# Performance work log

Hardware: AMD Instinct MI355X
Metric: run time of the kernel (lower is better)

## Reference

```python
import jax, jax.numpy as jnp
import numpy as np

N, E, G = 50000, 600000, 256
IN_C, EMB, HID, OUT = 64, 128, 128, 36


def _glorot(key, fan_in, fan_out):
    lim = np.sqrt(6.0 / (fan_in + fan_out)).astype(np.float32)
    return jax.random.uniform(key, (fan_in, fan_out), jnp.float32, -lim, lim)


def setup_inputs() -> dict:
    key = jax.random.key(0)
    ks = jax.random.split(key, 12)
    x = jax.random.normal(ks[0], (N, IN_C), jnp.float32)
    edge_index = jax.random.randint(ks[1], (2, E), 0, N, jnp.int64)
    edge_attr = jax.random.uniform(ks[2], (E,), jnp.float32)
    # deterministic sorted batch assignment -> every graph id 0..G-1 is nonempty
    batch = ((jnp.arange(N, dtype=jnp.int64) * G) // N).astype(jnp.int64)
    rho = jax.random.uniform(ks[3], (G,), jnp.float32)
    return {
        "x": x,
        "edge_attr": edge_attr,
        "rho": rho,
        "conv0_w": _glorot(ks[4], IN_C, EMB),
        "conv0_b": jnp.zeros((EMB,), jnp.float32),
        "conv1_w": _glorot(ks[5], EMB, EMB),
        "conv1_b": jnp.zeros((EMB,), jnp.float32),
        "mlp0_w": _glorot(ks[6], 2 * EMB + 1, HID),
        "mlp0_b": jnp.zeros((HID,), jnp.float32),
        "mlp1_w": _glorot(ks[7], HID, HID),
        "mlp1_b": jnp.zeros((HID,), jnp.float32),
        "out_w": _glorot(ks[8], HID, OUT),
        "out_b": jnp.zeros((OUT,), jnp.float32),
        "edge_index": edge_index,
        "batch": batch,
    }


def _gcn_conv(h, row, col, w, W, b):
    # PyG GCNConv: self-loops already appended in (row, col, w).
    deg = jax.ops.segment_sum(w, col, num_segments=N)  # in-degree by edge weight
    dis = jnp.where(deg > 0, jax.lax.rsqrt(jnp.maximum(deg, 1e-30)), 0.0)
    norm = dis[row] * w * dis[col]                     # [E+N]
    h = h @ W                                          # [N, out]
    msg = norm[:, None] * h[row]                       # gather + scale
    return jax.ops.segment_sum(msg, col, num_segments=N) + b


def reference(x, edge_attr, rho, conv0_w, conv0_b, conv1_w, conv1_b,
              mlp0_w, mlp0_b, mlp1_w, mlp1_b, out_w, out_b,
              edge_index, batch):
    # add self-loops with weight 1
    loops = jnp.arange(N, dtype=edge_index.dtype)
    row = jnp.concatenate([edge_index[0], loops])
    col = jnp.concatenate([edge_index[1], loops])
    w = jnp.concatenate([edge_attr, jnp.ones((N,), edge_attr.dtype)])

    h = jax.nn.relu(_gcn_conv(x, row, col, w, conv0_w, conv0_b))
    h = jax.nn.relu(_gcn_conv(h, row, col, w, conv1_w, conv1_b))

    gmp = jax.ops.segment_max(h, batch, num_segments=G)             # [G, EMB]
    cnt = jax.ops.segment_sum(jnp.ones((N,), h.dtype), batch, num_segments=G)
    gap = jax.ops.segment_sum(h, batch, num_segments=G) / cnt[:, None]
    hg = jnp.concatenate([gmp, gap, rho[:, None]], axis=1)          # [G, 2*EMB+1]

    hg = jax.nn.relu(hg @ mlp0_w + mlp0_b)
    hg = jax.nn.relu(hg @ mlp1_w + mlp1_b)
    return hg @ out_w + out_b
```

## Files before the change

### kernel.cpp

```cpp
#include <hip/hip_runtime.h>
#include <hip/hip_fp16.h>
#include <math.h>

using half8 = __attribute__((ext_vector_type(8))) _Float16;
using f32x4 = __attribute__((ext_vector_type(4))) float;

#define CAP 64


__device__ __forceinline__ float4 ld_half4(const __half* p) {
    int2 raw = *reinterpret_cast<const int2*>(p);
    __half2 a = *reinterpret_cast<__half2*>(&raw.x);
    __half2 b = *reinterpret_cast<__half2*>(&raw.y);
    return make_float4(__low2float(a), __high2float(a), __low2float(b), __high2float(b));
}

__device__ __forceinline__ void st_half4(__half* p, float4 v) {
    __half2 a = __floats2half2_rn(v.x, v.y);
    __half2 b = __floats2half2_rn(v.z, v.w);
    int2 raw;
    raw.x = *reinterpret_cast<int*>(&a);
    raw.y = *reinterpret_cast<int*>(&b);
    *reinterpret_cast<int2*>(p) = raw;
}


__global__ void k_wcvt(const float* __restrict__ w0, __half* __restrict__ wt0,
                       const float* __restrict__ w1, __half* __restrict__ wt1) {
    int idx = blockIdx.x * blockDim.x + threadIdx.x;
    if (idx < 64 * 128) {
        int k = idx >> 7, c = idx & 127;
        wt0[c * 64 + k] = __float2half(w0[idx]);
    } else if (idx < 64 * 128 + 128 * 128) {
        int i2 = idx - 64 * 128;
        int k = i2 >> 7, c = i2 & 127;
        wt1[c * 128 + k] = __float2half(w1[i2]);
    }
}


__global__ void k_init(int* cursor, int n) {
    int i = blockIdx.x * blockDim.x + threadIdx.x;
    if (i < n) cursor[i] = 0;
}

__global__ void k_place(const int* __restrict__ row, const int* __restrict__ col,
                        const float* __restrict__ w, int* __restrict__ cursor,
                        int2* __restrict__ slab, int e) {
    int base = (blockIdx.x * blockDim.x + threadIdx.x) * 4;
    if (base + 3 < e) {
        int4 r4 = *reinterpret_cast<const int4*>(&row[base]);
        int4 c4 = *reinterpret_cast<const int4*>(&col[base]);
        float4 w4 = *reinterpret_cast<const float4*>(&w[base]);
        int s0 = atomicAdd(&cursor[c4.x], 1);
        int s1 = atomicAdd(&cursor[c4.y], 1);
        int s2 = atomicAdd(&cursor[c4.z], 1);
        int s3 = atomicAdd(&cursor[c4.w], 1);
        if (s0 < CAP) slab[(size_t)c4.x * CAP + s0] = make_int2(r4.x, __float_as_int(w4.x));
        if (s1 < CAP) slab[(size_t)c4.y * CAP + s1] = make_int2(r4.y, __float_as_int(w4.y));
        if (s2 < CAP) slab[(size_t)c4.z * CAP + s2] = make_int2(r4.z, __float_as_int(w4.z));
        if (s3 < CAP) slab[(size_t)c4.w * CAP + s3] = make_int2(r4.w, __float_as_int(w4.w));
    } else {
        for (int i = base; i < e; ++i) {
            int c = col[i];
            int s = atomicAdd(&cursor[c], 1);
            if (s < CAP) slab[(size_t)c * CAP + s] = make_int2(row[i], __float_as_int(w[i]));
        }
    }
}

__global__ __launch_bounds__(256) void k_degscale(
    const int2* __restrict__ slab, const int* __restrict__ cursor,
    const float* __restrict__ x, float* __restrict__ dis,
    __half* __restrict__ xs, int n)
{
    __shared__ float sdis[256];
    int t = threadIdx.x;
    int base = blockIdx.x * 256;
    int i = base + t;
    if (i < n) {
        int cnt = min(cursor[i], CAP);
        float s = 1.0f;
        const int2* p = &slab[(size_t)i * CAP];
        for (int j = 0; j < cnt; ++j) s += __int_as_float(p[j].y);
        float d = rsqrtf(s);
        dis[i] = d;
        sdis[t] = d;
    }
    __syncthreads();
#pragma unroll
    for (int it = 0; it < 16; ++it) {
        int id = it * 256 + t;
        int node_l = id >> 4;
        if (base + node_l < n) {
            float d = sdis[node_l];
            float4 v = reinterpret_cast<const float4*>(x)[(size_t)base * 16 + id];
            v.x *= d; v.y *= d; v.z *= d; v.w *= d;
            st_half4(&xs[((size_t)base * 16 + id) * 4], v);
        }
    }
}


template<int COLS, int LPN>
__global__ __launch_bounds__(256) void k_agg(
    const __half* __restrict__ hs, const int2* __restrict__ slab,
    const int* __restrict__ cursor, const float* __restrict__ dis,
    __half* __restrict__ out, int n)
{
    int t = blockIdx.x * blockDim.x + threadIdx.x;
    int node = t / LPN, lane = t % LPN;
    if (node >= n) return;
    int c4 = lane * 4;
    float4 acc = ld_half4(&hs[(size_t)node * COLS + c4]);
    int beg = node * CAP;
    int end = beg + min(cursor[node], CAP);
    int p = beg;
    for (; p + 4 <= end; p += 4) {
        int2 e0 = slab[p], e1 = slab[p + 1], e2 = slab[p + 2], e3 = slab[p + 3];
        float w0 = __int_as_float(e0.y), w1 = __int_as_float(e1.y);
        float w2 = __int_as_float(e2.y), w3 = __int_as_float(e3.y);
        float4 v0 = ld_half4(&hs[(size_t)e0.x * COLS + c4]);
        float4 v1 = ld_half4(&hs[(size_t)e1.x * COLS + c4]);
        float4 v2 = ld_half4(&hs[(size_t)e2.x * COLS + c4]);
        float4 v3 = ld_half4(&hs[(size_t)e3.x * COLS + c4]);
        acc.x = fmaf(w0, v0.x, acc.x); acc.y = fmaf(w0, v0.y, acc.y);
        acc.z = fmaf(w0, v0.z, acc.z); acc.w = fmaf(w0, v0.w, acc.w);
        acc.x = fmaf(w1, v1.x, acc.x); acc.y = fmaf(w1, v1.y, acc.y);
        acc.z = fmaf(w1, v1.z, acc.z); acc.w = fmaf(w1, v1.w, acc.w);
        acc.x = fmaf(w2, v2.x, acc.x); acc.y = fmaf(w2, v2.y, acc.y);
        acc.z = fmaf(w2, v2.z, acc.z); acc.w = fmaf(w2, v2.w, acc.w);
        acc.x = fmaf(w3, v3.x, acc.x); acc.y = fmaf(w3, v3.y, acc.y);
        acc.z = fmaf(w3, v3.z, acc.z); acc.w = fmaf(w3, v3.w, acc.w);
    }
    for (; p < end; ++p) {
        int2 e0 = slab[p];
        float w0 = __int_as_float(e0.y);
        float4 v0 = ld_half4(&hs[(size_t)e0.x * COLS + c4]);
        acc.x = fmaf(w0, v0.x, acc.x); acc.y = fmaf(w0, v0.y, acc.y);
        acc.z = fmaf(w0, v0.z, acc.z); acc.w = fmaf(w0, v0.w, acc.w);
    }
    float d = dis[node];
    float4 o;
    o.x = d * acc.x; o.y = d * acc.y; o.z = d * acc.z; o.w = d * acc.w;
    st_half4(&out[(size_t)node * COLS + c4], o);
}


template<int K, bool SC>
__global__ __launch_bounds__(256) void k_gemm_mfma(
    const __half* __restrict__ A, const __half* __restrict__ wt,
    const float* __restrict__ bias, const float* __restrict__ scale,
    __half* __restrict__ out, int n)
{
    constexpr int SA = K + 8;
    constexpr int CPR = K / 8;
    __shared__ _Float16 Al[64 * SA];
    __shared__ _Float16 Wl[128 * SA];
    const int tid = threadIdx.x;
    const int row0 = blockIdx.x * 64;

#pragma unroll
    for (int it = 0; it < (64 * CPR) / 256; ++it) {
        int id = tid + it * 256;
        int r = id / CPR, kc = id % CPR;
        int gr = row0 + r; if (gr >= n) gr = n - 1;
        int4 raw = *reinterpret_cast<const int4*>(&A[(size_t)gr * K + kc * 8]);
        *reinterpret_cast<int4*>(&Al[r * SA + kc * 8]) = raw;
    }
#pragma unroll
    for (int it = 0; it < (128 * CPR) / 256; ++it) {
        int id = tid + it * 256;
        int c = id / CPR, kc = id % CPR;
        int4 raw = *reinterpret_cast<const int4*>(&wt[(size_t)c * K + kc * 8]);
        *reinterpret_cast<int4*>(&Wl[c * SA + kc * 8]) = raw;
    }
    __syncthreads();

    const int l = tid & 63, w = tid >> 6;
    const int r = l & 15, kg = l >> 4;

    f32x4 acc[8];
#pragma unroll
    for (int ct = 0; ct < 8; ++ct) acc[ct] = (f32x4){0.f, 0.f, 0.f, 0.f};

#pragma unroll
    for (int kst = 0; kst < K / 32; ++kst) {
        half8 af = *reinterpret_cast<const half8*>(&Al[(16 * w + r) * SA + kst * 32 + kg * 8]);
#pragma unroll
        for (int ct = 0; ct < 8; ++ct) {
            half8 bf = *reinterpret_cast<const half8*>(&Wl[(16 * ct + r) * SA + kst * 32 + kg * 8]);
            acc[ct] = __builtin_amdgcn_mfma_f32_16x16x32_f16(af, bf, acc[ct], 0, 0, 0);
        }
    }

    float sc[4];
#pragma unroll
    for (int q = 0; q < 4; ++q) {
        int gr = row0 + 16 * w + kg * 4 + q;
        sc[q] = (SC && gr < n) ? scale[gr] : 1.0f;
    }
#pragma unroll
    for (int ct = 0; ct < 8; ++ct) {
        float bv = bias[16 * ct + r];
#pragma unroll
        for (int q = 0; q < 4; ++q) {
            int gr = row0 + 16 * w + kg * 4 + q;
            if (gr < n) {
                float v = fmaxf(acc[ct][q] + bv, 0.f);
                if constexpr (SC) v *= sc[q];
                out[(size_t)gr * 128 + 16 * ct + r] = __float2half(v);
            }
        }
    }
}


__device__ __forceinline__ int lowbound(const int* __restrict__ b, int n, int key) {
    int lo = 0, hi = n;
    while (lo < hi) { int mid = (lo + hi) >> 1; if (b[mid] < key) lo = mid + 1; else hi = mid; }
    return lo;
}

#define NSLICE 8

__global__ __launch_bounds__(128) void k_pool_part(
    const __half* __restrict__ h, const int* __restrict__ batch,
    float* __restrict__ part, int n)
{
    int g = blockIdx.x >> 3, s = blockIdx.x & (NSLICE - 1);
    int ch = threadIdx.x;
    __shared__ int sbeg, send;
    if (ch == 0) {
        sbeg = lowbound(batch, n, g);
        send = lowbound(batch, n, g + 1);
    }
    __syncthreads();
    float mx = -INFINITY, sm = 0.f;
    for (int i = sbeg + s; i < send; i += NSLICE) {
        float v = __half2float(h[(size_t)i * 128 + ch]);
        mx = fmaxf(mx, v);
        sm += v;
    }
    size_t base = ((size_t)g * NSLICE + s) * 256;
    part[base + ch] = mx;
    part[base + 128 + ch] = sm;
}


__global__ __launch_bounds__(256) void k_head_mlp(
    const float* __restrict__ part, const int* __restrict__ batch,
    const float* __restrict__ rho,
    const float* __restrict__ w0, const float* __restrict__ b0,
    const float* __restrict__ w1, const float* __restrict__ b1,
    const float* __restrict__ w2, const float* __restrict__ b2,
    float* __restrict__ out, int n)
{
    int g = blockIdx.x;
    int tid = threadIdx.x;
    int ch = tid & 127, half = tid >> 7;
    __shared__ float hg[257];
    __shared__ float t0[128];
    __shared__ float red[2][128];
    __shared__ int scnt;
    if (tid == 0) {
        int beg = lowbound(batch, n, g);
        int end = lowbound(batch, n, g + 1);
        scnt = end - beg;
        hg[256] = rho[g];
    }
    {
        float mx = -INFINITY, sm = 0.f;
        for (int s = half * (NSLICE / 2); s < (half + 1) * (NSLICE / 2); ++s) {
            size_t base = ((size_t)g * NSLICE + s) * 256;
            mx = fmaxf(mx, part[base + ch]);
            sm += part[base + 128 + ch];
        }
        red[half][ch] = mx;
        __syncthreads();
        if (half == 0) {
            float m2 = fmaxf(mx, red[1][ch]);
            hg[ch] = m2;
            red[0][ch] = sm;
        }
        __syncthreads();
        if (half == 1) red[1][ch] = sm + red[0][ch];
        __syncthreads();
        if (half == 0) hg[128 + ch] = red[1][ch] / (float)scnt;
        __syncthreads();
    }
    {
        float a = 0.f, b = 0.f;
        int j0 = half * 128;
        int jend = half ? 257 : 128;
        int j = j0;
        for (; j + 2 <= jend; j += 2) {
            a = fmaf(hg[j], w0[(size_t)j * 128 + ch], a);
            b = fmaf(hg[j + 1], w0[(size_t)(j + 1) * 128 + ch], b);
        }
        if (j < jend) a = fmaf(hg[j], w0[(size_t)j * 128 + ch], a);
        red[half][ch] = a + b;
        __syncthreads();
        if (half == 0) t0[ch] = fmaxf(red[0][ch] + red[1][ch] + b0[ch], 0.f);
        __syncthreads();
    }
    {
        float a = 0.f, b = 0.f;
        int j0 = half * 64;
        for (int j = j0; j < j0 + 64; j += 2) {
            a = fmaf(t0[j], w1[(size_t)j * 128 + ch], a);
            b = fmaf(t0[j + 1], w1[(size_t)(j + 1) * 128 + ch], b);
        }
        red[half][ch] = a + b;
        __syncthreads();
        if (half == 0) hg[ch] = fmaxf(red[0][ch] + red[1][ch] + b1[ch], 0.f);
        __syncthreads();
    }
    if (ch < 36) {
        float a = 0.f, b = 0.f;
        int j0 = half * 64;
        for (int j = j0; j < j0 + 64; j += 2) {
            a = fmaf(hg[j], w2[(size_t)j * 36 + ch], a);
            b = fmaf(hg[j + 1], w2[(size_t)(j + 1) * 36 + ch], b);
        }
        red[half][ch] = a + b;
    }
    __syncthreads();
    if (half == 0 && ch < 36)
        out[(size_t)g * 36 + ch] = red[0][ch] + red[1][ch] + b2[ch];
}


extern "C" void kernel_launch(void* const* d_in, const int* in_sizes, int n_in,
                              void* d_out, int out_size, void* d_ws, size_t ws_size,
                              hipStream_t stream)
{
    const float* x        = (const float*)d_in[0];
    const float* edge_attr= (const float*)d_in[1];
    const float* rho      = (const float*)d_in[2];
    const float* conv0_w  = (const float*)d_in[3];
    const float* conv0_b  = (const float*)d_in[4];
    const float* conv1_w  = (const float*)d_in[5];
    const float* conv1_b  = (const float*)d_in[6];
    const float* mlp0_w   = (const float*)d_in[7];
    const float* mlp0_b   = (const float*)d_in[8];
    const float* mlp1_w   = (const float*)d_in[9];
    const float* mlp1_b   = (const float*)d_in[10];
    const float* out_w    = (const float*)d_in[11];
    const float* out_b    = (const float*)d_in[12];
    const int*   edge_idx = (const int*)d_in[13];
    const int*   batch    = (const int*)d_in[14];

    const int N = in_sizes[0] / 64;
    const int E = in_sizes[1];
    const int G = in_sizes[2];
    const int* erow = edge_idx;
    const int* ecol = edge_idx + E;

    char* ws = (char*)d_ws;
    size_t off = 0;
    auto alloc = [&](size_t bytes) -> void* {
        off = (off + 255) & ~(size_t)255;
        void* p = ws + off;
        off += bytes;
        return p;
    };
    float*  dis    = (float*)alloc((size_t)N * 4);
    int*    cursor = (int*)  alloc((size_t)N * 4);
    int2*   slab   = (int2*) alloc((size_t)N * CAP * 8);
    __half* bufA   = (__half*)alloc((size_t)N * 128 * 2);
    __half* bufB   = (__half*)alloc((size_t)N * 128 * 2);
    float*  part   = (float*)alloc((size_t)G * NSLICE * 256 * 4);
    __half* wt0    = (__half*)alloc((size_t)64 * 128 * 2);
    __half* wt1    = (__half*)alloc((size_t)128 * 128 * 2);

    dim3 b256(256);
    k_wcvt<<<(64 * 128 + 128 * 128 + 255) / 256, b256, 0, stream>>>(conv0_w, wt0, conv1_w, wt1);
    k_init<<<(N + 255) / 256, b256, 0, stream>>>(cursor, N);
    k_place<<<((E + 3) / 4 + 255) / 256, b256, 0, stream>>>(erow, ecol, edge_attr, cursor, slab, E);
    k_degscale<<<(N + 255) / 256, b256, 0, stream>>>(slab, cursor, x, dis, bufA, N);

    k_agg<64, 16><<<((size_t)N * 16 + 255) / 256, b256, 0, stream>>>(bufA, slab, cursor, dis, bufB, N);
    k_gemm_mfma<64, true><<<(N + 63) / 64, b256, 0, stream>>>(bufB, wt0, conv0_b, dis, bufA, N);
    k_agg<128, 32><<<((size_t)N * 32 + 255) / 256, b256, 0, stream>>>(bufA, slab, cursor, dis, bufB, N);
    k_gemm_mfma<128, false><<<(N + 63) / 64, b256, 0, stream>>>(bufB, wt1, conv1_b, nullptr, bufA, N);

    k_pool_part<<<G * NSLICE, dim3(128), 0, stream>>>(bufA, batch, part, N);
    k_head_mlp<<<G, b256, 0, stream>>>(part, batch, rho,
                                       mlp0_w, mlp0_b, mlp1_w, mlp1_b, out_w, out_b,
                                       (float*)d_out, N);
}
```

Measured before the change: 169.1 us.

## Fuse neighbor aggregation into MFMA GEMM prologue and pack edge slab to 32-bit

Each GCN layer now runs its aggregation inside the GEMM kernel, 4 threads per node, writing straight into the LDS A-tile. This removes the separate aggregation kernels and the global round-trip of the intermediate feature buffer. Edge records are packed into 32 bits (16-bit source index plus fp16 weight), halving slab traffic, but this assumes fewer than 65536 nodes and lowers weight precision. The weight-conversion and cursor-init kernels are merged into one launch. The trade-off is less per-node gather parallelism and lower occupancy from the LDS-heavy fused kernel.

```diff
diff --git a/kernel.cpp b/kernel.cpp
--- a/kernel.cpp
+++ b/kernel.cpp
@@ -8,11 +8,16 @@
 #define CAP 64
 
 
-__device__ __forceinline__ float4 ld_half4(const __half* p) {
-    int2 raw = *reinterpret_cast<const int2*>(p);
-    __half2 a = *reinterpret_cast<__half2*>(&raw.x);
-    __half2 b = *reinterpret_cast<__half2*>(&raw.y);
-    return make_float4(__low2float(a), __high2float(a), __low2float(b), __high2float(b));
+__device__ __forceinline__ float wdec(unsigned int v) {
+    __half h;
+    *reinterpret_cast<unsigned short*>(&h) = (unsigned short)(v >> 16);
+    return __half2float(h);
+}
+
+__device__ __forceinline__ unsigned int wenc(int src, float w) {
+    __half h = __float2half(w);
+    return (unsigned int)src |
+           ((unsigned int)(*reinterpret_cast<unsigned short*>(&h)) << 16);
 }
 
 __device__ __forceinline__ void st_half4(__half* p, float4 v) {
@@ -25,28 +30,25 @@
 }
 
 
-__global__ void k_wcvt(const float* __restrict__ w0, __half* __restrict__ wt0,
-                       const float* __restrict__ w1, __half* __restrict__ wt1) {
-    int idx = blockIdx.x * blockDim.x + threadIdx.x;
-    if (idx < 64 * 128) {
-        int k = idx >> 7, c = idx & 127;
-        wt0[c * 64 + k] = __float2half(w0[idx]);
-    } else if (idx < 64 * 128 + 128 * 128) {
-        int i2 = idx - 64 * 128;
-        int k = i2 >> 7, c = i2 & 127;
-        wt1[c * 128 + k] = __float2half(w1[i2]);
-    }
-}
-
-
-__global__ void k_init(int* cursor, int n) {
+__global__ void k_setup(const float* __restrict__ w0, __half* __restrict__ wt0,
+                        const float* __restrict__ w1, __half* __restrict__ wt1,
+                        int* __restrict__ cursor, int n) {
     int i = blockIdx.x * blockDim.x + threadIdx.x;
+    if (i < 64 * 128) {
+        int k = i >> 7, c = i & 127;
+        wt0[c * 64 + k] = __float2half(w0[i]);
+    }
+    if (i < 128 * 128) {
+        int k = i >> 7, c = i & 127;
+        wt1[c * 128 + k] = __float2half(w1[i]);
+    }
     if (i < n) cursor[i] = 0;
 }
+
 
 __global__ void k_place(const int* __restrict__ row, const int* __restrict__ col,
                         const float* __restrict__ w, int* __restrict__ cursor,
-                        int2* __restrict__ slab, int e) {
+                        unsigned int* __restrict__ slab, int e) {
     int base = (blockIdx.x * blockDim.x + threadIdx.x) * 4;
     if (base + 3 < e) {
         int4 r4 = *reinterpret_cast<const int4*>(&row[base]);
@@ -56,21 +58,21 @@
         int s1 = atomicAdd(&cursor[c4.y], 1);
         int s2 = atomicAdd(&cursor[c4.z], 1);
         int s3 = atomicAdd(&cursor[c4.w], 1);
-        if (s0 < CAP) slab[(size_t)c4.x * CAP + s0] = make_int2(r4.x, __float_as_int(w4.x));
-        if (s1 < CAP) slab[(size_t)c4.y * CAP + s1] = make_int2(r4.y, __float_as_int(w4.y));
-        if (s2 < CAP) slab[(size_t)c4.z * CAP + s2] = make_int2(r4.z, __float_as_int(w4.z));
-        if (s3 < CAP) slab[(size_t)c4.w * CAP + s3] = make_int2(r4.w, __float_as_int(w4.w));
+        if (s0 < CAP) slab[(size_t)c4.x * CAP + s0] = wenc(r4.x, w4.x);
+        if (s1 < CAP) slab[(size_t)c4.y * CAP + s1] = wenc(r4.y, w4.y);
+        if (s2 < CAP) slab[(size_t)c4.z * CAP + s2] = wenc(r4.z, w4.z);
+        if (s3 < CAP) slab[(size_t)c4.w * CAP + s3] = wenc(r4.w, w4.w);
     } else {
         for (int i = base; i < e; ++i) {
             int c = col[i];
             int s = atomicAdd(&cursor[c], 1);
-            if (s < CAP) slab[(size_t)c * CAP + s] = make_int2(row[i], __float_as_int(w[i]));
+            if (s < CAP) slab[(size_t)c * CAP + s] = wenc(row[i], w[i]);
         }
     }
 }
 
 __global__ __launch_bounds__(256) void k_degscale(
-    const int2* __restrict__ slab, const int* __restrict__ cursor,
+    const unsigned int* __restrict__ slab, const int* __restrict__ cursor,
     const float* __restrict__ x, float* __restrict__ dis,
     __half* __restrict__ xs, int n)
 {
@@ -81,8 +83,8 @@
     if (i < n) {
         int cnt = min(cursor[i], CAP);
         float s = 1.0f;
-        const int2* p = &slab[(size_t)i * CAP];
-        for (int j = 0; j < cnt; ++j) s += __int_as_float(p[j].y);
+        const unsigned int* p = &slab[(size_t)i * CAP];
+        for (int j = 0; j < cnt; ++j) s += wdec(p[j]);
         float d = rsqrtf(s);
         dis[i] = d;
         sdis[t] = d;
@@ -102,72 +104,21 @@
 }
 
 
-template<int COLS, int LPN>
-__global__ __launch_bounds__(256) void k_agg(
-    const __half* __restrict__ hs, const int2* __restrict__ slab,
+template<int K, bool SC>
+__global__ __launch_bounds__(256) void k_agg_gemm(
+    const __half* __restrict__ hs, const unsigned int* __restrict__ slab,
     const int* __restrict__ cursor, const float* __restrict__ dis,
-    __half* __restrict__ out, int n)
-{
-    int t = blockIdx.x * blockDim.x + threadIdx.x;
-    int node = t / LPN, lane = t % LPN;
-    if (node >= n) return;
-    int c4 = lane * 4;
-    float4 acc = ld_half4(&hs[(size_t)node * COLS + c4]);
-    int beg = node * CAP;
-    int end = beg + min(cursor[node], CAP);
-    int p = beg;
-    for (; p + 4 <= end; p += 4) {
-        int2 e0 = slab[p], e1 = slab[p + 1], e2 = slab[p + 2], e3 = slab[p + 3];
-        float w0 = __int_as_float(e0.y), w1 = __int_as_float(e1.y);
-        float w2 = __int_as_float(e2.y), w3 = __int_as_float(e3.y);
-        float4 v0 = ld_half4(&hs[(size_t)e0.x * COLS + c4]);
-        float4 v1 = ld_half4(&hs[(size_t)e1.x * COLS + c4]);
-        float4 v2 = ld_half4(&hs[(size_t)e2.x * COLS + c4]);
-        float4 v3 = ld_half4(&hs[(size_t)e3.x * COLS + c4]);
-        acc.x = fmaf(w0, v0.x, acc.x); acc.y = fmaf(w0, v0.y, acc.y);
-        acc.z = fmaf(w0, v0.z, acc.z); acc.w = fmaf(w0, v0.w, acc.w);
-        acc.x = fmaf(w1, v1.x, acc.x); acc.y = fmaf(w1, v1.y, acc.y);
-        acc.z = fmaf(w1, v1.z, acc.z); acc.w = fmaf(w1, v1.w, acc.w);
-        acc.x = fmaf(w2, v2.x, acc.x); acc.y = fmaf(w2, v2.y, acc.y);
-        acc.z = fmaf(w2, v2.z, acc.z); acc.w = fmaf(w2, v2.w, acc.w);
-        acc.x = fmaf(w3, v3.x, acc.x); acc.y = fmaf(w3, v3.y, acc.y);
-        acc.z = fmaf(w3, v3.z, acc.z); acc.w = fmaf(w3, v3.w, acc.w);
-    }
-    for (; p < end; ++p) {
-        int2 e0 = slab[p];
-        float w0 = __int_as_float(e0.y);
-        float4 v0 = ld_half4(&hs[(size_t)e0.x * COLS + c4]);
-        acc.x = fmaf(w0, v0.x, acc.x); acc.y = fmaf(w0, v0.y, acc.y);
-        acc.z = fmaf(w0, v0.z, acc.z); acc.w = fmaf(w0, v0.w, acc.w);
-    }
-    float d = dis[node];
-    float4 o;
-    o.x = d * acc.x; o.y = d * acc.y; o.z = d * acc.z; o.w = d * acc.w;
-    st_half4(&out[(size_t)node * COLS + c4], o);
-}
-
-
-template<int K, bool SC>
-__global__ __launch_bounds__(256) void k_gemm_mfma(
-    const __half* __restrict__ A, const __half* __restrict__ wt,
-    const float* __restrict__ bias, const float* __restrict__ scale,
+    const __half* __restrict__ wt, const float* __restrict__ bias,
     __half* __restrict__ out, int n)
 {
     constexpr int SA = K + 8;
     constexpr int CPR = K / 8;
+    constexpr int CW = K / 4;
     __shared__ _Float16 Al[64 * SA];
     __shared__ _Float16 Wl[128 * SA];
     const int tid = threadIdx.x;
     const int row0 = blockIdx.x * 64;
 
-#pragma unroll
-    for (int it = 0; it < (64 * CPR) / 256; ++it) {
-        int id = tid + it * 256;
-        int r = id / CPR, kc = id % CPR;
-        int gr = row0 + r; if (gr >= n) gr = n - 1;
-        int4 raw = *reinterpret_cast<const int4*>(&A[(size_t)gr * K + kc * 8]);
-        *reinterpret_cast<int4*>(&Al[r * SA + kc * 8]) = raw;
-    }
 #pragma unroll
     for (int it = 0; it < (128 * CPR) / 256; ++it) {
         int id = tid + it * 256;
@@ -175,6 +126,43 @@
         int4 raw = *reinterpret_cast<const int4*>(&wt[(size_t)c * K + kc * 8]);
         *reinterpret_cast<int4*>(&Wl[c * SA + kc * 8]) = raw;
     }
+
+    {
+        const int lr = tid >> 2, part = tid & 3;
+        const int node = row0 + lr;
+        const int c0 = part * CW;
+        if (node < n) {
+            float acc[CW];
+#pragma unroll
+            for (int cc = 0; cc < CW / 8; ++cc) {
+                half8 v = *reinterpret_cast<const half8*>(&hs[(size_t)node * K + c0 + cc * 8]);
+#pragma unroll
+                for (int u = 0; u < 8; ++u) acc[cc * 8 + u] = (float)v[u];
+            }
+            int cnt = min(cursor[node], CAP);
+            const unsigned int* sp = &slab[(size_t)node * CAP];
+            for (int j = 0; j < cnt; ++j) {
+                unsigned int rec = sp[j];
+                int src = rec & 0xFFFF;
+                float w = wdec(rec);
+#pragma unroll
+                for (int cc = 0; cc < CW / 8; ++cc) {
+                    half8 v = *reinterpret_cast<const half8*>(&hs[(size_t)src * K + c0 + cc * 8]);
+#pragma unroll
+                    for (int u = 0; u < 8; ++u)
+                        acc[cc * 8 + u] = fmaf(w, (float)v[u], acc[cc * 8 + u]);
+                }
+            }
+            float d = dis[node];
+#pragma unroll
+            for (int cc = 0; cc < CW / 8; ++cc) {
+                half8 hv;
+#pragma unroll
+                for (int u = 0; u < 8; ++u) hv[u] = (_Float16)(d * acc[cc * 8 + u]);
+                *reinterpret_cast<half8*>(&Al[lr * SA + c0 + cc * 8]) = hv;
+            }
+        }
+    }
     __syncthreads();
 
     const int l = tid & 63, w = tid >> 6;
@@ -198,7 +186,7 @@
 #pragma unroll
     for (int q = 0; q < 4; ++q) {
         int gr = row0 + 16 * w + kg * 4 + q;
-        sc[q] = (SC && gr < n) ? scale[gr] : 1.0f;
+        sc[q] = (SC && gr < n) ? dis[gr] : 1.0f;
     }
 #pragma unroll
     for (int ct = 0; ct < 8; ++ct) {
@@ -365,25 +353,23 @@
         off += bytes;
         return p;
     };
-    float*  dis    = (float*)alloc((size_t)N * 4);
-    int*    cursor = (int*)  alloc((size_t)N * 4);
-    int2*   slab   = (int2*) alloc((size_t)N * CAP * 8);
-    __half* bufA   = (__half*)alloc((size_t)N * 128 * 2);
-    __half* bufB   = (__half*)alloc((size_t)N * 128 * 2);
-    float*  part   = (float*)alloc((size_t)G * NSLICE * 256 * 4);
-    __half* wt0    = (__half*)alloc((size_t)64 * 128 * 2);
-    __half* wt1    = (__half*)alloc((size_t)128 * 128 * 2);
+    float*        dis    = (float*)alloc((size_t)N * 4);
+    int*          cursor = (int*)  alloc((size_t)N * 4);
+    unsigned int* slab   = (unsigned int*)alloc((size_t)N * CAP * 4);
+    __half*       bufA   = (__half*)alloc((size_t)N * 128 * 2);
+    __half*       bufB   = (__half*)alloc((size_t)N * 128 * 2);
+    float*        part   = (float*)alloc((size_t)G * NSLICE * 256 * 4);
+    __half*       wt0    = (__half*)alloc((size_t)64 * 128 * 2);
+    __half*       wt1    = (__half*)alloc((size_t)128 * 128 * 2);
 
     dim3 b256(256);
-    k_wcvt<<<(64 * 128 + 128 * 128 + 255) / 256, b256, 0, stream>>>(conv0_w, wt0, conv1_w, wt1);
-    k_init<<<(N + 255) / 256, b256, 0, stream>>>(cursor, N);
+    int setup_n = (N > 128 * 128) ? N : 128 * 128;
+    k_setup<<<(setup_n + 255) / 256, b256, 0, stream>>>(conv0_w, wt0, conv1_w, wt1, cursor, N);
     k_place<<<((E + 3) / 4 + 255) / 256, b256, 0, stream>>>(erow, ecol, edge_attr, cursor, slab, E);
     k_degscale<<<(N + 255) / 256, b256, 0, stream>>>(slab, cursor, x, dis, bufA, N);
 
-    k_agg<64, 16><<<((size_t)N * 16 + 255) / 256, b256, 0, stream>>>(bufA, slab, cursor, dis, bufB, N);
-    k_gemm_mfma<64, true><<<(N + 63) / 64, b256, 0, stream>>>(bufB, wt0, conv0_b, dis, bufA, N);
-    k_agg<128, 32><<<((size_t)N * 32 + 255) / 256, b256, 0, stream>>>(bufA, slab, cursor, dis, bufB, N);
-    k_gemm_mfma<128, false><<<(N + 63) / 64, b256, 0, stream>>>(bufB, wt1, conv1_b, nullptr, bufA, N);
+    k_agg_gemm<64, true><<<(N + 63) / 64, b256, 0, stream>>>(bufA, slab, cursor, dis, wt0, conv0_b, bufB, N);
+    k_agg_gemm<128, false><<<(N + 63) / 64, b256, 0, stream>>>(bufB, slab, cursor, dis, wt1, conv1_b, bufA, N);
 
     k_pool_part<<<G * NSLICE, dim3(128), 0, stream>>>(bufA, batch, part, N);
     k_head_mlp<<<G, b256, 0, stream>>>(part, batch, rho,
```

Result: no change. 166.6 us (-1.5%).
